# Performance work log

Hardware: AMD Instinct MI355X
Metric: run time of the kernel (lower is better)

## Reference

```python
import jax, jax.numpy as jnp
import numpy as np
import math

N_HEADS = 8
D_E = 64


def setup_inputs() -> dict:
    key = jax.random.key(0)
    k1, k2, k3 = jax.random.split(key, 3)
    B, C, L = 4, 512, 2048
    x = jax.random.normal(k1, (B, C, L), dtype=jnp.float32)
    # 1x1-conv (channel-mixing) projection shared by Q and K (the original
    # uses query_conv for both Q and K).
    W_q = jax.random.normal(k2, (N_HEADS * D_E, C), dtype=jnp.float32) * 0.02
    b_q = jax.random.normal(k3, (N_HEADS * D_E,), dtype=jnp.float32) * 0.02
    return {"x": x, "W_q": W_q, "b_q": b_q}


def reference(x, W_q, b_q):
    B, C, L = x.shape
    H, d_e = N_HEADS, D_E
    # 1x1 conv over channels: (B, H*d_e, L)
    qk = jnp.einsum('oc,bcl->bol', W_q, x) + b_q[None, :, None]
    # (B, H, L, d_e); K == Q per the original (both use query_conv)
    Q = qk.reshape(B, H, d_e, L).transpose(0, 1, 3, 2)
    K = Q
    scores = jnp.einsum('bhqd,bhkd->bhqk', Q, K) / math.sqrt(d_e)
    # causal mask: positions k > q masked to -inf (triu(diagonal=1) masked)
    causal = jnp.arange(L)[None, :] <= jnp.arange(L)[:, None]  # (L, L)
    scores = jnp.where(causal[None, None], scores, -jnp.inf)
    A = jax.nn.softmax(scores, axis=-1)  # (B, H, L, L)
    # values are the raw input sequence, (B, L, C)
    V = x.transpose(0, 2, 1)
    H_att = jnp.einsum('bhqk,bkc->bhqc', A, V)  # (B, H, L, C)
    out = H_att + V[:, None]                      # residual add per head
    # -> (B, H*C, L)
    return out.transpose(0, 1, 3, 2).reshape(B, H * C, L)
```

## Files before the change

### kernel.cpp

```cpp
#include <hip/hip_runtime.h>
#include <hip/hip_bf16.h>

#define B_ 4
#define C_ 512
#define L_ 2048
#define H_ 8
#define E_ 64
#define QSCALE 0.4246609f
#define NUNITS_B 256

typedef __attribute__((ext_vector_type(8))) short bf16x8;
typedef __attribute__((ext_vector_type(4))) float f32x4;
typedef __attribute__((ext_vector_type(4))) unsigned short u16x4;

static __device__ __forceinline__ unsigned short f2bf(float f) {
    union { float f; unsigned u; } v; v.f = f;
    unsigned r = v.u + 0x7FFFu + ((v.u >> 16) & 1u);
    return (unsigned short)(r >> 16);
}

#define LBAR() do { asm volatile("s_waitcnt lgkmcnt(0)" ::: "memory"); \
                    __builtin_amdgcn_s_barrier(); } while (0)

__global__ __launch_bounds__(256) void prep_kernel(const float* __restrict__ x,
                                                   unsigned short* __restrict__ xb,
                                                   unsigned short* __restrict__ xt) {
    const int lt = blockIdx.x, ct = blockIdx.y, b = blockIdx.z;
    const int l0 = lt * 64, c0 = ct * 64;
    const int t = threadIdx.x;
    __shared__ unsigned short T[64 * 72];

    const int cl = t >> 2, lo = (t & 3) * 16;
    const float* src = x + ((size_t)(b * C_ + c0 + cl)) * L_ + l0 + lo;
    unsigned short u[16];
    #pragma unroll
    for (int j = 0; j < 16; j += 4) {
        float4 v = *reinterpret_cast<const float4*>(src + j);
        u[j] = f2bf(v.x); u[j + 1] = f2bf(v.y); u[j + 2] = f2bf(v.z); u[j + 3] = f2bf(v.w);
    }
    unsigned short* xbp = xb + ((size_t)(b * C_ + c0 + cl)) * L_ + l0 + lo;
    reinterpret_cast<uint4*>(xbp)[0] = reinterpret_cast<uint4*>(u)[0];
    reinterpret_cast<uint4*>(xbp)[1] = reinterpret_cast<uint4*>(u)[1];
    reinterpret_cast<uint4*>(&T[cl * 72 + lo])[0] = reinterpret_cast<uint4*>(u)[0];
    reinterpret_cast<uint4*>(&T[cl * 72 + lo + 8])[0] = reinterpret_cast<uint4*>(u)[1];
    __syncthreads();
    const int ll = t >> 2, co = (t & 3) * 16;
    unsigned short v16[16];
    #pragma unroll
    for (int j = 0; j < 16; ++j) v16[j] = T[(co + j) * 72 + ll];
    unsigned short* xtp = xt + ((size_t)b * L_ + l0 + ll) * C_ + c0 + co;
    reinterpret_cast<uint4*>(xtp)[0] = reinterpret_cast<uint4*>(v16)[0];
    reinterpret_cast<uint4*>(xtp)[1] = reinterpret_cast<uint4*>(v16)[1];
}

__global__ __launch_bounds__(256) void wcast_kernel(const float* __restrict__ W,
                                                    unsigned short* __restrict__ Wb) {
    const int i = blockIdx.x * 256 + threadIdx.x;
    float4 v = reinterpret_cast<const float4*>(W)[i];
    union { unsigned short u[4]; unsigned long long ll; } o;
    o.u[0] = f2bf(v.x); o.u[1] = f2bf(v.y); o.u[2] = f2bf(v.z); o.u[3] = f2bf(v.w);
    reinterpret_cast<unsigned long long*>(Wb)[i] = o.ll;
}

__global__ __launch_bounds__(256) void proj_kernel(const unsigned short* __restrict__ Wb,
                                                   const float* __restrict__ bq,
                                                   const unsigned short* __restrict__ xt,
                                                   unsigned short* __restrict__ qb) {
    const int lt = blockIdx.x, h = blockIdx.y, b = blockIdx.z;
    const int tid = threadIdx.x, w = tid >> 6, lane = tid & 63;
    const int lr = lane & 15, lg = lane >> 4;
    const int l = lt * 64 + w * 16 + lr;
    const int o0 = h * 64;

    f32x4 acc[4] = {};
    const unsigned short* xrow = xt + ((size_t)b * L_ + l) * C_;
    for (int ks = 0; ks < 16; ++ks) {
        bf16x8 bf = *reinterpret_cast<const bf16x8*>(xrow + ks * 32 + lg * 8);
        #pragma unroll
        for (int mt = 0; mt < 4; ++mt) {
            bf16x8 af = *reinterpret_cast<const bf16x8*>(Wb + (size_t)(o0 + mt * 16 + lr) * C_ + ks * 32 + lg * 8);
            acc[mt] = __builtin_amdgcn_mfma_f32_16x16x32_bf16(af, bf, acc[mt], 0, 0, 0);
        }
    }
    const int bh = b * H_ + h;
    unsigned short* qrow = qb + ((size_t)bh * L_ + l) * 64;
    #pragma unroll
    for (int mt = 0; mt < 4; ++mt) {
        const int e0 = mt * 16 + lg * 4;
        const float4 bb = *reinterpret_cast<const float4*>(bq + o0 + e0);
        union { unsigned short u[4]; unsigned long long ll; } o;
        o.u[0] = f2bf((acc[mt][0] + bb.x) * QSCALE);
        o.u[1] = f2bf((acc[mt][1] + bb.y) * QSCALE);
        o.u[2] = f2bf((acc[mt][2] + bb.z) * QSCALE);
        o.u[3] = f2bf((acc[mt][3] + bb.w) * QSCALE);
        *reinterpret_cast<unsigned long long*>(qrow + e0) = o.ll;
    }
}

#define LDVB(BK, KOFF)                                                                  \
    {                                                                                   \
        _Pragma("unroll")                                                               \
        for (int ct = 0; ct < 4; ++ct)                                                  \
            pvv[BK][ct] = *reinterpret_cast<const bf16x8*>(                             \
                Vbase + (size_t)(c0w + ct * 16 + lr) * L_ + (KOFF) + lg * 8);           \
    }

#define PV_STEP(CUR, NXT, S_)                                                           \
    {                                                                                   \
        const int s_ = (S_);                                                            \
        if (s_ + 2 < ksmax) LDVB(NXT, k0 + (s_ + 2) * 32)                               \
        bf16x8 pa[4];                                                                   \
        _Pragma("unroll")                                                               \
        for (int mt = 0; mt < 4; ++mt) {                                                \
            const int row = mt * 16 + lr;                                               \
            const int g2 = (s_ * 4 + lg) ^ (lr & 7);                                    \
            pa[mt] = *reinterpret_cast<const bf16x8*>(&P[row * 512 + (g2 << 3)]);       \
        }                                                                               \
        __builtin_amdgcn_s_setprio(1);                                                  \
        _Pragma("unroll")                                                               \
        for (int mt = 0; mt < 4; ++mt)                                                  \
            _Pragma("unroll")                                                           \
            for (int ct = 0; ct < 4; ++ct)                                              \
                acc[mt][ct] = __builtin_amdgcn_mfma_f32_16x16x32_bf16(                  \
                    pa[mt], pvv[CUR][ct], acc[mt][ct], 0, 0, 0);                        \
        __builtin_amdgcn_s_setprio(0);                                                  \
    }

__global__ __launch_bounds__(512, 2) void pv_kernel(const unsigned short* __restrict__ qb,
                                                    const unsigned short* __restrict__ xb,
                                                    float* __restrict__ out,
                                                    int* __restrict__ counters) {
    const int tid = threadIdx.x, w = tid >> 6, lane = tid & 63;
    const int lr = lane & 15, lg = lane >> 4;
    const int c0w = w * 64;
    const int myb = (blockIdx.x & 7) >> 1;

    __shared__ unsigned short Qt[64 * 64];
    __shared__ unsigned short P[64 * 512];
    __shared__ float rsT[64][8];
    __shared__ int s_u;

    const int b = myb;
    const unsigned short* Vbase = xb + (size_t)b * C_ * L_;

    for (;;) {
        __syncthreads();
        if (tid == 0) s_u = atomicAdd(counters + myb, 1);
        __syncthreads();
        const int u = s_u;
        if (u >= NUNITS_B) return;

        const int qt = 31 - (u >> 3);
        const int h = u & 7;
        const int q0 = qt * 64, qlim = q0 + 63;
        const int nkt = (q0 >> 9) + 1;
        const int bh = b * H_ + h;
        const unsigned short* Qbase = qb + (size_t)bh * L_ * 64;

        {
            const int r = tid >> 3, g = tid & 7;
            bf16x8 v = *reinterpret_cast<const bf16x8*>(Qbase + (size_t)(q0 + r) * 64 + g * 8);
            *reinterpret_cast<bf16x8*>(&Qt[r * 64 + ((g ^ (r & 7)) << 3)]) = v;
        }

        bf16x8 pvv[4][4];
        f32x4 acc[4][4] = {};
        float rs[4] = {0.f, 0.f, 0.f, 0.f};

        LBAR();

        #pragma unroll 1
        for (int kt = 0; kt < nkt; ++kt) {
            const int k0 = kt * 512;
            const int ksmax = min(16, ((qlim - k0) >> 5) + 1);
            const int kw0 = k0 + w * 64;

            if (kw0 <= qlim) {
                bf16x8 kb[4][2];
                #pragma unroll
                for (int ksub = 0; ksub < 4; ++ksub) {
                    const size_t krow = (size_t)(kw0 + ksub * 16 + lr) * 64;
                    kb[ksub][0] = *reinterpret_cast<const bf16x8*>(Qbase + krow + lg * 8);
                    kb[ksub][1] = *reinterpret_cast<const bf16x8*>(Qbase + krow + 32 + lg * 8);
                }
                LDVB(0, k0)
                LDVB(1, k0 + 32)
                #pragma unroll
                for (int nt = 0; nt < 4; ++nt) {
                    const int qrow = nt * 16 + lr;
                    bf16x8 aq0 = *reinterpret_cast<const bf16x8*>(&Qt[qrow * 64 + ((lg ^ (lr & 7)) << 3)]);
                    bf16x8 aq1 = *reinterpret_cast<const bf16x8*>(&Qt[qrow * 64 + (((4 + lg) ^ (lr & 7)) << 3)]);
                    const int q = q0 + qrow;
                    #pragma unroll
                    for (int ksub = 0; ksub < 4; ++ksub) {
                        f32x4 z = {};
                        z = __builtin_amdgcn_mfma_f32_16x16x32_bf16(kb[ksub][0], aq0, z, 0, 0, 0);
                        z = __builtin_amdgcn_mfma_f32_16x16x32_bf16(kb[ksub][1], aq1, z, 0, 0, 0);
                        const int kbase = kw0 + ksub * 16 + lg * 4;
                        const float p0 = (kbase + 0 <= q) ? exp2f(z[0]) : 0.f;
                        const float p1 = (kbase + 1 <= q) ? exp2f(z[1]) : 0.f;
                        const float p2 = (kbase + 2 <= q) ? exp2f(z[2]) : 0.f;
                        const float p3 = (kbase + 3 <= q) ? exp2f(z[3]) : 0.f;
                        rs[nt] += (p0 + p1) + (p2 + p3);
                        unsigned r01, r23;
                        asm("v_cvt_pk_bf16_f32 %0, %1, %2" : "=v"(r01) : "v"(p0), "v"(p1));
                        asm("v_cvt_pk_bf16_f32 %0, %1, %2" : "=v"(r23) : "v"(p2), "v"(p3));
                        const int kl = w * 64 + ksub * 16 + lg * 4;
                        const int gg = (kl >> 3) ^ (qrow & 7);
                        const unsigned long long pk = ((unsigned long long)r23 << 32) | r01;
                        *reinterpret_cast<unsigned long long*>(&P[qrow * 512 + (gg << 3) + (kl & 7)]) = pk;
                    }
                }
            } else {
                LDVB(0, k0)
                LDVB(1, k0 + 32)
            }
            LBAR();

            int s = 0;
            #pragma unroll 1
            for (; s + 4 <= ksmax; s += 4) {
                PV_STEP(0, 2, s)
                PV_STEP(1, 3, s + 1)
                PV_STEP(2, 0, s + 2)
                PV_STEP(3, 1, s + 3)
            }
            if (s < ksmax) {
                PV_STEP(0, 2, s)
                PV_STEP(1, 3, s + 1)
            }
            LBAR();
        }

        #pragma unroll
        for (int nt = 0; nt < 4; ++nt) {
            float t0 = __shfl_xor(rs[nt], 16); rs[nt] += t0;
            float t1 = __shfl_xor(rs[nt], 32); rs[nt] += t1;
        }
        if (lg == 0) {
            #pragma unroll
            for (int nt = 0; nt < 4; ++nt) rsT[nt * 16 + lr][w] = rs[nt];
        }
        LBAR();

        const unsigned short* xres = xb + (size_t)b * C_ * L_;
        float* ob = out + (size_t)bh * C_ * L_;
        #pragma unroll
        for (int mt = 0; mt < 4; ++mt) {
            f32x4 li;
            #pragma unroll
            for (int r = 0; r < 4; ++r) {
                const f32x4 s0 = *reinterpret_cast<const f32x4*>(&rsT[mt * 16 + lg * 4 + r][0]);
                const f32x4 s1 = *reinterpret_cast<const f32x4*>(&rsT[mt * 16 + lg * 4 + r][4]);
                li[r] = 1.f / (((s0[0] + s0[1]) + (s0[2] + s0[3])) + ((s1[0] + s1[1]) + (s1[2] + s1[3])));
            }
            const int lbase = q0 + mt * 16 + lg * 4;
            #pragma unroll
            for (int ct = 0; ct < 4; ++ct) {
                const int c = c0w + ct * 16 + lr;
                const u16x4 rv = __builtin_nontemporal_load(
                    reinterpret_cast<const u16x4*>(xres + (size_t)c * L_ + lbase));
                f32x4 o;
                o[0] = acc[mt][ct][0] * li[0] + __uint_as_float((unsigned)rv[0] << 16);
                o[1] = acc[mt][ct][1] * li[1] + __uint_as_float((unsigned)rv[1] << 16);
                o[2] = acc[mt][ct][2] * li[2] + __uint_as_float((unsigned)rv[2] << 16);
                o[3] = acc[mt][ct][3] * li[3] + __uint_as_float((unsigned)rv[3] << 16);
                __builtin_nontemporal_store(o, reinterpret_cast<f32x4*>(ob + (size_t)c * L_ + lbase));
            }
        }
    }
}

extern "C" void kernel_launch(void* const* d_in, const int* in_sizes, int n_in,
                              void* d_out, int out_size, void* d_ws, size_t ws_size,
                              hipStream_t stream) {
    const float* x  = (const float*)d_in[0];
    const float* Wq = (const float*)d_in[1];
    const float* bq = (const float*)d_in[2];
    float* out = (float*)d_out;

    unsigned short* xb   = (unsigned short*)d_ws;
    unsigned short* xt   = xb + (size_t)B_ * C_ * L_;
    unsigned short* qbuf = xt + (size_t)B_ * L_ * C_;
    unsigned short* Wb   = qbuf + (size_t)B_ * H_ * L_ * E_;
    int* counters = (int*)(Wb + (size_t)H_ * E_ * C_);

    (void)hipMemsetAsync(counters, 0, 16, stream);
    prep_kernel<<<dim3(32, 8, 4), 256, 0, stream>>>(x, xb, xt);
    wcast_kernel<<<dim3(256), 256, 0, stream>>>(Wq, Wb);
    proj_kernel<<<dim3(32, 8, 4), 256, 0, stream>>>(Wb, bq, xt, qbuf);
    pv_kernel<<<dim3(512), 512, 0, stream>>>(qbuf, xb, out, counters);
}
```

Baseline: 251.8 us.

## Raise occupancy, shrink V prefetch buffers, specialize unmasked score tiles

The PV kernel's launch bound goes from 2 to 4 blocks per SM, and the V register double-buffer shrinks from 4 stages to 2, cutting register pressure. The score phase now has an unmasked variant for tiles wholly below the diagonal and uses the hardware exp2 builtin. Full 512-wide key tiles get a fully unrolled PV loop. The intent is more latency hiding through occupancy and less mask and exp overhead. The risks are a shorter V prefetch distance, possible register spills under the tighter bound, and LDS usage that may not actually allow 4 blocks.

After: 442.6 us. +75.8%, slower.

```diff
diff --git a/kernel.cpp b/kernel.cpp
--- a/kernel.cpp
+++ b/kernel.cpp
@@ -105,15 +105,14 @@
                 Vbase + (size_t)(c0w + ct * 16 + lr) * L_ + (KOFF) + lg * 8);           \
     }
 
-#define PV_STEP(CUR, NXT, S_)                                                           \
+#define PV_STEP(CUR, NXT, S_, KSMAX_)                                                   \
     {                                                                                   \
-        const int s_ = (S_);                                                            \
-        if (s_ + 2 < ksmax) LDVB(NXT, k0 + (s_ + 2) * 32)                               \
+        if ((S_) + 1 < (KSMAX_)) LDVB(NXT, k0 + ((S_) + 1) * 32)                        \
         bf16x8 pa[4];                                                                   \
         _Pragma("unroll")                                                               \
         for (int mt = 0; mt < 4; ++mt) {                                                \
             const int row = mt * 16 + lr;                                               \
-            const int g2 = (s_ * 4 + lg) ^ (lr & 7);                                    \
+            const int g2 = ((S_) * 4 + lg) ^ (lr & 7);                                  \
             pa[mt] = *reinterpret_cast<const bf16x8*>(&P[row * 512 + (g2 << 3)]);       \
         }                                                                               \
         __builtin_amdgcn_s_setprio(1);                                                  \
@@ -126,7 +125,52 @@
         __builtin_amdgcn_s_setprio(0);                                                  \
     }
 
-__global__ __launch_bounds__(512, 2) void pv_kernel(const unsigned short* __restrict__ qb,
+#define S_PHASE(MASKED)                                                                          \
+    {                                                                                            \
+        bf16x8 kb[4][2];                                                                         \
+        _Pragma("unroll")                                                                        \
+        for (int ksub = 0; ksub < 4; ++ksub) {                                                   \
+            const size_t krow = (size_t)(kw0 + ksub * 16 + lr) * 64;                             \
+            kb[ksub][0] = *reinterpret_cast<const bf16x8*>(Qbase + krow + lg * 8);               \
+            kb[ksub][1] = *reinterpret_cast<const bf16x8*>(Qbase + krow + 32 + lg * 8);          \
+        }                                                                                        \
+        _Pragma("unroll")                                                                        \
+        for (int nt = 0; nt < 4; ++nt) {                                                         \
+            const int qrow = nt * 16 + lr;                                                       \
+            bf16x8 aq0 = *reinterpret_cast<const bf16x8*>(&Qt[qrow * 64 + ((lg ^ (lr & 7)) << 3)]);        \
+            bf16x8 aq1 = *reinterpret_cast<const bf16x8*>(&Qt[qrow * 64 + (((4 + lg) ^ (lr & 7)) << 3)]);  \
+            const int q = q0 + qrow;                                                             \
+            _Pragma("unroll")                                                                    \
+            for (int ksub = 0; ksub < 4; ++ksub) {                                               \
+                f32x4 z = {};                                                                    \
+                z = __builtin_amdgcn_mfma_f32_16x16x32_bf16(kb[ksub][0], aq0, z, 0, 0, 0);       \
+                z = __builtin_amdgcn_mfma_f32_16x16x32_bf16(kb[ksub][1], aq1, z, 0, 0, 0);       \
+                float p0, p1, p2, p3;                                                            \
+                if (MASKED) {                                                                    \
+                    const int kbase = kw0 + ksub * 16 + lg * 4;                                  \
+                    p0 = (kbase + 0 <= q) ? __builtin_amdgcn_exp2f(z[0]) : 0.f;                  \
+                    p1 = (kbase + 1 <= q) ? __builtin_amdgcn_exp2f(z[1]) : 0.f;                  \
+                    p2 = (kbase + 2 <= q) ? __builtin_amdgcn_exp2f(z[2]) : 0.f;                  \
+                    p3 = (kbase + 3 <= q) ? __builtin_amdgcn_exp2f(z[3]) : 0.f;                  \
+                } else {                                                                         \
+                    p0 = __builtin_amdgcn_exp2f(z[0]);                                           \
+                    p1 = __builtin_amdgcn_exp2f(z[1]);                                           \
+                    p2 = __builtin_amdgcn_exp2f(z[2]);                                           \
+                    p3 = __builtin_amdgcn_exp2f(z[3]);                                           \
+                }                                                                                \
+                rs[nt] += (p0 + p1) + (p2 + p3);                                                 \
+                unsigned r01, r23;                                                               \
+                asm("v_cvt_pk_bf16_f32 %0, %1, %2" : "=v"(r01) : "v"(p0), "v"(p1));              \
+                asm("v_cvt_pk_bf16_f32 %0, %1, %2" : "=v"(r23) : "v"(p2), "v"(p3));              \
+                const int kl = w * 64 + ksub * 16 + lg * 4;                                      \
+                const int gg = (kl >> 3) ^ (qrow & 7);                                           \
+                const unsigned long long pk = ((unsigned long long)r23 << 32) | r01;             \
+                *reinterpret_cast<unsigned long long*>(&P[qrow * 512 + (gg << 3) + (kl & 7)]) = pk; \
+            }                                                                                    \
+        }                                                                                        \
+    }
+
+__global__ __launch_bounds__(512, 4) void pv_kernel(const unsigned short* __restrict__ qb,
                                                     const unsigned short* __restrict__ xb,
                                                     float* __restrict__ out,
                                                     int* __restrict__ counters) {
@@ -163,7 +207,7 @@
             *reinterpret_cast<bf16x8*>(&Qt[r * 64 + ((g ^ (r & 7)) << 3)]) = v;
         }
 
-        bf16x8 pvv[4][4];
+        bf16x8 pvv[2][4];
         f32x4 acc[4][4] = {};
         float rs[4] = {0.f, 0.f, 0.f, 0.f};
 
@@ -175,59 +219,26 @@
             const int ksmax = min(16, ((qlim - k0) >> 5) + 1);
             const int kw0 = k0 + w * 64;
 
-            if (kw0 <= qlim) {
-                bf16x8 kb[4][2];
+            LDVB(0, k0)
+
+            if (kw0 + 63 < q0) {
+                S_PHASE(0)
+            } else if (kw0 <= qlim) {
+                S_PHASE(1)
+            }
+            LBAR();
+
+            if (ksmax == 16) {
                 #pragma unroll
-                for (int ksub = 0; ksub < 4; ++ksub) {
-                    const size_t krow = (size_t)(kw0 + ksub * 16 + lr) * 64;
-                    kb[ksub][0] = *reinterpret_cast<const bf16x8*>(Qbase + krow + lg * 8);
-                    kb[ksub][1] = *reinterpret_cast<const bf16x8*>(Qbase + krow + 32 + lg * 8);
-                }
-                LDVB(0, k0)
-                LDVB(1, k0 + 32)
-                #pragma unroll
-                for (int nt = 0; nt < 4; ++nt) {
-                    const int qrow = nt * 16 + lr;
-                    bf16x8 aq0 = *reinterpret_cast<const bf16x8*>(&Qt[qrow * 64 + ((lg ^ (lr & 7)) << 3)]);
-                    bf16x8 aq1 = *reinterpret_cast<const bf16x8*>(&Qt[qrow * 64 + (((4 + lg) ^ (lr & 7)) << 3)]);
-                    const int q = q0 + qrow;
-                    #pragma unroll
-                    for (int ksub = 0; ksub < 4; ++ksub) {
-                        f32x4 z = {};
-                        z = __builtin_amdgcn_mfma_f32_16x16x32_bf16(kb[ksub][0], aq0, z, 0, 0, 0);
-                        z = __builtin_amdgcn_mfma_f32_16x16x32_bf16(kb[ksub][1], aq1, z, 0, 0, 0);
-                        const int kbase = kw0 + ksub * 16 + lg * 4;
-                        const float p0 = (kbase + 0 <= q) ? exp2f(z[0]) : 0.f;
-                        const float p1 = (kbase + 1 <= q) ? exp2f(z[1]) : 0.f;
-                        const float p2 = (kbase + 2 <= q) ? exp2f(z[2]) : 0.f;
-                        const float p3 = (kbase + 3 <= q) ? exp2f(z[3]) : 0.f;
-                        rs[nt] += (p0 + p1) + (p2 + p3);
-                        unsigned r01, r23;
-                        asm("v_cvt_pk_bf16_f32 %0, %1, %2" : "=v"(r01) : "v"(p0), "v"(p1));
-                        asm("v_cvt_pk_bf16_f32 %0, %1, %2" : "=v"(r23) : "v"(p2), "v"(p3));
-                        const int kl = w * 64 + ksub * 16 + lg * 4;
-                        const int gg = (kl >> 3) ^ (qrow & 7);
-                        const unsigned long long pk = ((unsigned long long)r23 << 32) | r01;
-                        *reinterpret_cast<unsigned long long*>(&P[qrow * 512 + (gg << 3) + (kl & 7)]) = pk;
-                    }
+                for (int s = 0; s < 16; ++s) {
+                    PV_STEP(s & 1, (s + 1) & 1, s, 16)
                 }
             } else {
-                LDVB(0, k0)
-                LDVB(1, k0 + 32)
-            }
-            LBAR();
-
-            int s = 0;
-            #pragma unroll 1
-            for (; s + 4 <= ksmax; s += 4) {
-                PV_STEP(0, 2, s)
-                PV_STEP(1, 3, s + 1)
-                PV_STEP(2, 0, s + 2)
-                PV_STEP(3, 1, s + 3)
-            }
-            if (s < ksmax) {
-                PV_STEP(0, 2, s)
-                PV_STEP(1, 3, s + 1)
+                #pragma unroll 1
+                for (int s = 0; s < ksmax; s += 2) {
+                    PV_STEP(0, 1, s, ksmax)
+                    PV_STEP(1, 0, s + 1, ksmax)
+                }
             }
             LBAR();
         }
```

## Restructure attention kernel into single-wave 16-row units with per-wave channel halves

Applied to the files above, without the earlier changes.

The attention/PV kernel changes from 512-thread blocks handling 64 query rows with shared P staging and block barriers to single-wave blocks. Each wave handles 16 query rows and half of the channels, and takes work units from an atomic per-batch queue (2048 units). Block-wide barriers go away, fewer whole-tile causal-masked evaluations are wasted, and the 64-wide key tile has an unmasked fast path. In exchange, V tiles are reused across only 16 query rows instead of 64, so global/L2 traffic for V rises, and S is recomputed for each channel half.

Result: slower. 674.9 us (+168.1%).

```diff
diff --git a/kernel.cpp b/kernel.cpp
--- a/kernel.cpp
+++ b/kernel.cpp
@@ -7,7 +7,7 @@
 #define H_ 8
 #define E_ 64
 #define QSCALE 0.4246609f
-#define NUNITS_B 256
+#define NUNITS_B 2048
 
 typedef __attribute__((ext_vector_type(8))) short bf16x8;
 typedef __attribute__((ext_vector_type(4))) float f32x4;
@@ -18,9 +18,6 @@
     unsigned r = v.u + 0x7FFFu + ((v.u >> 16) & 1u);
     return (unsigned short)(r >> 16);
 }
-
-#define LBAR() do { asm volatile("s_waitcnt lgkmcnt(0)" ::: "memory"); \
-                    __builtin_amdgcn_s_barrier(); } while (0)
 
 __global__ __launch_bounds__(256) void prep_kernel(const float* __restrict__ x,
                                                    unsigned short* __restrict__ xb,
@@ -97,176 +94,144 @@
     }
 }
 
-#define LDVB(BK, KOFF)                                                                  \
+
+#define LDVG(BK, G)                                                                     \
     {                                                                                   \
         _Pragma("unroll")                                                               \
-        for (int ct = 0; ct < 4; ++ct)                                                  \
-            pvv[BK][ct] = *reinterpret_cast<const bf16x8*>(                             \
-                Vbase + (size_t)(c0w + ct * 16 + lr) * L_ + (KOFF) + lg * 8);           \
-    }
-
-#define PV_STEP(CUR, NXT, S_)                                                           \
+        for (int c4 = 0; c4 < 4; ++c4)                                                  \
+            vf[BK][c4] = *reinterpret_cast<const bf16x8*>(                              \
+                Vbase + (size_t)(c0w + ((G) & 3) * 64 + c4 * 16 + lr) * L_              \
+                      + k0 + ((G) >> 2) * 32 + lg * 8);                                 \
+    }
+
+#define PVG(BK, G)                                                                      \
     {                                                                                   \
-        const int s_ = (S_);                                                            \
-        if (s_ + 2 < ksmax) LDVB(NXT, k0 + (s_ + 2) * 32)                               \
-        bf16x8 pa[4];                                                                   \
         _Pragma("unroll")                                                               \
-        for (int mt = 0; mt < 4; ++mt) {                                                \
-            const int row = mt * 16 + lr;                                               \
-            const int g2 = (s_ * 4 + lg) ^ (lr & 7);                                    \
-            pa[mt] = *reinterpret_cast<const bf16x8*>(&P[row * 512 + (g2 << 3)]);       \
+        for (int c4 = 0; c4 < 4; ++c4)                                                  \
+            acc[((G) & 3) * 4 + c4] = __builtin_amdgcn_mfma_f32_16x16x32_bf16(          \
+                pa[(G) >> 2], vf[BK][c4], acc[((G) & 3) * 4 + c4], 0, 0, 0);            \
+    }
+
+#define S_SUB(S2, MASKED)                                                               \
+    {                                                                                   \
+        f32x4 z = {};                                                                   \
+        z = __builtin_amdgcn_mfma_f32_16x16x32_bf16(kb[S2][0], qf0, z, 0, 0, 0);        \
+        z = __builtin_amdgcn_mfma_f32_16x16x32_bf16(kb[S2][1], qf1, z, 0, 0, 0);        \
+        float p0, p1, p2, p3;                                                           \
+        if (MASKED) {                                                                   \
+            const int kbase = k0 + (S2) * 16 + lg * 4;                                  \
+            p0 = (kbase + 0 <= q) ? __builtin_amdgcn_exp2f(z[0]) : 0.f;                 \
+            p1 = (kbase + 1 <= q) ? __builtin_amdgcn_exp2f(z[1]) : 0.f;                 \
+            p2 = (kbase + 2 <= q) ? __builtin_amdgcn_exp2f(z[2]) : 0.f;                 \
+            p3 = (kbase + 3 <= q) ? __builtin_amdgcn_exp2f(z[3]) : 0.f;                 \
+        } else {                                                                        \
+            p0 = __builtin_amdgcn_exp2f(z[0]);                                          \
+            p1 = __builtin_amdgcn_exp2f(z[1]);                                          \
+            p2 = __builtin_amdgcn_exp2f(z[2]);                                          \
+            p3 = __builtin_amdgcn_exp2f(z[3]);                                          \
         }                                                                               \
-        __builtin_amdgcn_s_setprio(1);                                                  \
-        _Pragma("unroll")                                                               \
-        for (int mt = 0; mt < 4; ++mt)                                                  \
-            _Pragma("unroll")                                                           \
-            for (int ct = 0; ct < 4; ++ct)                                              \
-                acc[mt][ct] = __builtin_amdgcn_mfma_f32_16x16x32_bf16(                  \
-                    pa[mt], pvv[CUR][ct], acc[mt][ct], 0, 0, 0);                        \
-        __builtin_amdgcn_s_setprio(0);                                                  \
-    }
-
-__global__ __launch_bounds__(512, 2) void pv_kernel(const unsigned short* __restrict__ qb,
-                                                    const unsigned short* __restrict__ xb,
-                                                    float* __restrict__ out,
-                                                    int* __restrict__ counters) {
-    const int tid = threadIdx.x, w = tid >> 6, lane = tid & 63;
+        rs += (p0 + p1) + (p2 + p3);                                                    \
+        unsigned r01, r23;                                                              \
+        asm("v_cvt_pk_bf16_f32 %0, %1, %2" : "=v"(r01) : "v"(p0), "v"(p1));             \
+        asm("v_cvt_pk_bf16_f32 %0, %1, %2" : "=v"(r23) : "v"(p2), "v"(p3));             \
+        const unsigned long long pk = ((unsigned long long)r23 << 32) | r01;            \
+        *reinterpret_cast<unsigned long long*>(&P[lr * 72 + (S2) * 16 + lg * 4]) = pk;  \
+    }
+
+__global__ __launch_bounds__(64, 2) void pv_kernel(const unsigned short* __restrict__ qb,
+                                                   const unsigned short* __restrict__ xb,
+                                                   float* __restrict__ out,
+                                                   int* __restrict__ counters) {
+    const int lane = threadIdx.x;
     const int lr = lane & 15, lg = lane >> 4;
-    const int c0w = w * 64;
     const int myb = (blockIdx.x & 7) >> 1;
 
-    __shared__ unsigned short Qt[64 * 64];
-    __shared__ unsigned short P[64 * 512];
-    __shared__ float rsT[64][8];
-    __shared__ int s_u;
+    __shared__ unsigned short P[16 * 72];
 
     const int b = myb;
     const unsigned short* Vbase = xb + (size_t)b * C_ * L_;
+    const unsigned short* xres = xb + (size_t)b * C_ * L_;
 
     for (;;) {
-        __syncthreads();
-        if (tid == 0) s_u = atomicAdd(counters + myb, 1);
-        __syncthreads();
-        const int u = s_u;
+        int u0;
+        if (lane == 0) u0 = atomicAdd(counters + myb, 1);
+        const int u = __shfl(u0, 0);
         if (u >= NUNITS_B) return;
 
-        const int qt = 31 - (u >> 3);
-        const int h = u & 7;
-        const int q0 = qt * 64, qlim = q0 + 63;
-        const int nkt = (q0 >> 9) + 1;
+        const int qt16 = 127 - (u >> 4);
+        const int h = (u >> 1) & 7;
+        const int chalf = u & 1;
+        const int q0 = qt16 * 16, qlim = q0 + 15;
+        const int q = q0 + lr;
+        const int nkt = (qt16 >> 2) + 1;
+        const int c0w = chalf * 256;
         const int bh = b * H_ + h;
         const unsigned short* Qbase = qb + (size_t)bh * L_ * 64;
 
-        {
-            const int r = tid >> 3, g = tid & 7;
-            bf16x8 v = *reinterpret_cast<const bf16x8*>(Qbase + (size_t)(q0 + r) * 64 + g * 8);
-            *reinterpret_cast<bf16x8*>(&Qt[r * 64 + ((g ^ (r & 7)) << 3)]) = v;
-        }
-
-        bf16x8 pvv[4][4];
-        f32x4 acc[4][4] = {};
-        float rs[4] = {0.f, 0.f, 0.f, 0.f};
-
-        LBAR();
+        const bf16x8 qf0 = *reinterpret_cast<const bf16x8*>(Qbase + (size_t)(q0 + lr) * 64 + lg * 8);
+        const bf16x8 qf1 = *reinterpret_cast<const bf16x8*>(Qbase + (size_t)(q0 + lr) * 64 + 32 + lg * 8);
+
+        f32x4 acc[16] = {};
+        float rs = 0.f;
+        bf16x8 vf[2][4];
 
         #pragma unroll 1
         for (int kt = 0; kt < nkt; ++kt) {
-            const int k0 = kt * 512;
-            const int ksmax = min(16, ((qlim - k0) >> 5) + 1);
-            const int kw0 = k0 + w * 64;
-
-            if (kw0 <= qlim) {
-                bf16x8 kb[4][2];
-                #pragma unroll
-                for (int ksub = 0; ksub < 4; ++ksub) {
-                    const size_t krow = (size_t)(kw0 + ksub * 16 + lr) * 64;
-                    kb[ksub][0] = *reinterpret_cast<const bf16x8*>(Qbase + krow + lg * 8);
-                    kb[ksub][1] = *reinterpret_cast<const bf16x8*>(Qbase + krow + 32 + lg * 8);
-                }
-                LDVB(0, k0)
-                LDVB(1, k0 + 32)
-                #pragma unroll
-                for (int nt = 0; nt < 4; ++nt) {
-                    const int qrow = nt * 16 + lr;
-                    bf16x8 aq0 = *reinterpret_cast<const bf16x8*>(&Qt[qrow * 64 + ((lg ^ (lr & 7)) << 3)]);
-                    bf16x8 aq1 = *reinterpret_cast<const bf16x8*>(&Qt[qrow * 64 + (((4 + lg) ^ (lr & 7)) << 3)]);
-                    const int q = q0 + qrow;
-                    #pragma unroll
-                    for (int ksub = 0; ksub < 4; ++ksub) {
-                        f32x4 z = {};
-                        z = __builtin_amdgcn_mfma_f32_16x16x32_bf16(kb[ksub][0], aq0, z, 0, 0, 0);
-                        z = __builtin_amdgcn_mfma_f32_16x16x32_bf16(kb[ksub][1], aq1, z, 0, 0, 0);
-                        const int kbase = kw0 + ksub * 16 + lg * 4;
-                        const float p0 = (kbase + 0 <= q) ? exp2f(z[0]) : 0.f;
-                        const float p1 = (kbase + 1 <= q) ? exp2f(z[1]) : 0.f;
-                        const float p2 = (kbase + 2 <= q) ? exp2f(z[2]) : 0.f;
-                        const float p3 = (kbase + 3 <= q) ? exp2f(z[3]) : 0.f;
-                        rs[nt] += (p0 + p1) + (p2 + p3);
-                        unsigned r01, r23;
-                        asm("v_cvt_pk_bf16_f32 %0, %1, %2" : "=v"(r01) : "v"(p0), "v"(p1));
-                        asm("v_cvt_pk_bf16_f32 %0, %1, %2" : "=v"(r23) : "v"(p2), "v"(p3));
-                        const int kl = w * 64 + ksub * 16 + lg * 4;
-                        const int gg = (kl >> 3) ^ (qrow & 7);
-                        const unsigned long long pk = ((unsigned long long)r23 << 32) | r01;
-                        *reinterpret_cast<unsigned long long*>(&P[qrow * 512 + (gg << 3) + (kl & 7)]) = pk;
-                    }
-                }
+            const int k0 = kt * 64;
+
+            bf16x8 kb[4][2];
+            #pragma unroll
+            for (int s2 = 0; s2 < 4; ++s2) {
+                const size_t krow = (size_t)(k0 + s2 * 16 + lr) * 64;
+                kb[s2][0] = *reinterpret_cast<const bf16x8*>(Qbase + krow + lg * 8);
+                kb[s2][1] = *reinterpret_cast<const bf16x8*>(Qbase + krow + 32 + lg * 8);
+            }
+
+            if (k0 + 63 <= q0) {
+                S_SUB(0, 0) S_SUB(1, 0) S_SUB(2, 0) S_SUB(3, 0)
             } else {
-                LDVB(0, k0)
-                LDVB(1, k0 + 32)
+                S_SUB(0, 1) S_SUB(1, 1) S_SUB(2, 1) S_SUB(3, 1)
             }
-            LBAR();
-
-            int s = 0;
-            #pragma unroll 1
-            for (; s + 4 <= ksmax; s += 4) {
-                PV_STEP(0, 2, s)
-                PV_STEP(1, 3, s + 1)
-                PV_STEP(2, 0, s + 2)
-                PV_STEP(3, 1, s + 3)
+
+            bf16x8 pa[2];
+            pa[0] = *reinterpret_cast<const bf16x8*>(&P[lr * 72 + lg * 8]);
+            pa[1] = *reinterpret_cast<const bf16x8*>(&P[lr * 72 + 32 + lg * 8]);
+
+            const bool full = (k0 + 32 <= qlim);
+            LDVG(0, 0)
+            LDVG(1, 1) PVG(0, 0)
+            LDVG(0, 2) PVG(1, 1)
+            LDVG(1, 3) PVG(0, 2)
+            if (full) {
+                LDVG(0, 4) PVG(1, 3)
+                LDVG(1, 5) PVG(0, 4)
+                LDVG(0, 6) PVG(1, 5)
+                LDVG(1, 7) PVG(0, 6)
+                PVG(1, 7)
+            } else {
+                PVG(1, 3)
             }
-            if (s < ksmax) {
-                PV_STEP(0, 2, s)
-                PV_STEP(1, 3, s + 1)
-            }
-            LBAR();
         }
 
+        rs += __shfl_xor(rs, 16);
+        rs += __shfl_xor(rs, 32);
+        f32x4 li;
         #pragma unroll
-        for (int nt = 0; nt < 4; ++nt) {
-            float t0 = __shfl_xor(rs[nt], 16); rs[nt] += t0;
-            float t1 = __shfl_xor(rs[nt], 32); rs[nt] += t1;
-        }
-        if (lg == 0) {
-            #pragma unroll
-            for (int nt = 0; nt < 4; ++nt) rsT[nt * 16 + lr][w] = rs[nt];
-        }
-        LBAR();
-
-        const unsigned short* xres = xb + (size_t)b * C_ * L_;
+        for (int r = 0; r < 4; ++r) li[r] = 1.f / __shfl(rs, lg * 4 + r);
+
         float* ob = out + (size_t)bh * C_ * L_;
+        const int lbase = q0 + lg * 4;
         #pragma unroll
-        for (int mt = 0; mt < 4; ++mt) {
-            f32x4 li;
-            #pragma unroll
-            for (int r = 0; r < 4; ++r) {
-                const f32x4 s0 = *reinterpret_cast<const f32x4*>(&rsT[mt * 16 + lg * 4 + r][0]);
-                const f32x4 s1 = *reinterpret_cast<const f32x4*>(&rsT[mt * 16 + lg * 4 + r][4]);
-                li[r] = 1.f / (((s0[0] + s0[1]) + (s0[2] + s0[3])) + ((s1[0] + s1[1]) + (s1[2] + s1[3])));
-            }
-            const int lbase = q0 + mt * 16 + lg * 4;
-            #pragma unroll
-            for (int ct = 0; ct < 4; ++ct) {
-                const int c = c0w + ct * 16 + lr;
-                const u16x4 rv = __builtin_nontemporal_load(
-                    reinterpret_cast<const u16x4*>(xres + (size_t)c * L_ + lbase));
-                f32x4 o;
-                o[0] = acc[mt][ct][0] * li[0] + __uint_as_float((unsigned)rv[0] << 16);
-                o[1] = acc[mt][ct][1] * li[1] + __uint_as_float((unsigned)rv[1] << 16);
-                o[2] = acc[mt][ct][2] * li[2] + __uint_as_float((unsigned)rv[2] << 16);
-                o[3] = acc[mt][ct][3] * li[3] + __uint_as_float((unsigned)rv[3] << 16);
-                __builtin_nontemporal_store(o, reinterpret_cast<f32x4*>(ob + (size_t)c * L_ + lbase));
-            }
+        for (int ct = 0; ct < 16; ++ct) {
+            const int c = c0w + ct * 16 + lr;
+            const u16x4 rv = __builtin_nontemporal_load(
+                reinterpret_cast<const u16x4*>(xres + (size_t)c * L_ + lbase));
+            f32x4 o;
+            o[0] = acc[ct][0] * li[0] + __uint_as_float((unsigned)rv[0] << 16);
+            o[1] = acc[ct][1] * li[1] + __uint_as_float((unsigned)rv[1] << 16);
+            o[2] = acc[ct][2] * li[2] + __uint_as_float((unsigned)rv[2] << 16);
+            o[3] = acc[ct][3] * li[3] + __uint_as_float((unsigned)rv[3] << 16);
+            __builtin_nontemporal_store(o, reinterpret_cast<f32x4*>(ob + (size_t)c * L_ + lbase));
         }
     }
 }
@@ -289,5 +254,5 @@
     prep_kernel<<<dim3(32, 8, 4), 256, 0, stream>>>(x, xb, xt);
     wcast_kernel<<<dim3(256), 256, 0, stream>>>(Wq, Wb);
     proj_kernel<<<dim3(32, 8, 4), 256, 0, stream>>>(Wb, bq, xt, qbuf);
-    pv_kernel<<<dim3(512), 512, 0, stream>>>(qbuf, xb, out, counters);
-}
+    pv_kernel<<<dim3(2048), 64, 0, stream>>>(qbuf, xb, out, counters);
+}
```
